# Kernel optimization log

Measured on AMD Instinct MI355X. Metric: run time of the kernel, lower is better.

The kernel has to match this reference:

```python
import jax, jax.numpy as jnp
import numpy as np

C = 1.0          # Poincare ball curvature
H = 8            # num_heads
EPS = 1e-15
DELTA = 1e-7
SC = np.sqrt(C)  # sqrt curvature


def _norm(x):
    return jnp.sqrt(jnp.clip(jnp.sum(x * x, -1, keepdims=True), 1e-15))


def mobius_add(x, y):
    xy = jnp.sum(x * y, -1, keepdims=True)
    x2 = jnp.sum(x * x, -1, keepdims=True)
    y2 = jnp.sum(y * y, -1, keepdims=True)
    num = (1 + 2 * C * xy + C * y2) * x + (1 - C * x2) * y
    den = 1 + 2 * C * xy + C * C * x2 * y2
    return num / (den + EPS)


def mobius_matvec(W, x):
    xn = _norm(x)
    mx = x @ W.T
    mxn = _norm(mx)
    arg = jnp.clip(SC * xn, None, 1 - 1e-5)
    return jnp.tanh(mxn / xn * jnp.arctanh(arg)) * mx / (mxn * SC)


def logmap0(x):
    xn = _norm(x)
    return jnp.arctanh(jnp.clip(SC * xn, None, 1 - 1e-5)) * x / (SC * xn)


def expmap0(u):
    un = _norm(u)
    return jnp.tanh(SC * un) * u / (SC * un)


def hyp_linear(W, b, x):
    return mobius_add(mobius_matvec(W, x), b)


def setup_inputs() -> dict:
    key = jax.random.key(0)
    ks = jax.random.split(key, 5)
    B, S, E = 2, 512, 256
    x = jax.random.normal(ks[0], (B, S, E), jnp.float32) * 0.02  # inside unit ball
    scale = float(np.sqrt(6.0 / (E + E)))  # xavier uniform bound
    Wq = jax.random.uniform(ks[1], (E, E), jnp.float32, -scale, scale)
    Wk = jax.random.uniform(ks[2], (E, E), jnp.float32, -scale, scale)
    Wv = jax.random.uniform(ks[3], (E, E), jnp.float32, -scale, scale)
    Wo = jax.random.uniform(ks[4], (E, E), jnp.float32, -scale, scale)
    z = jnp.zeros((E,), jnp.float32)
    head_scaling = jnp.ones((H, 1, 1), jnp.float32)
    return {"x": x, "Wq": Wq, "bq": z, "Wk": Wk, "bk": z, "Wv": Wv, "bv": z,
            "Wo": Wo, "bo": z, "head_scaling": head_scaling}


def reference(x, Wq, bq, Wk, bk, Wv, bv, Wo, bo, head_scaling):
    B, S, E = x.shape
    D = E // H
    q = hyp_linear(Wq, bq, x).reshape(B, S, H, D).transpose(0, 2, 1, 3)  # (B,H,S,D)
    k = hyp_linear(Wk, bk, x).reshape(B, S, H, D).transpose(0, 2, 1, 3)
    v = hyp_linear(Wv, bv, x).reshape(B, S, H, D).transpose(0, 2, 1, 3)
    max_norm = (1 - 1e-5) / SC
    q = jnp.minimum(q, max_norm)  # elementwise clamp_max, faithful to source
    k = jnp.minimum(k, max_norm)
    qn = C * jnp.sum(q * q, -1)[..., :, None]   # (B,H,Sq,1)
    kn = C * jnp.sum(k * k, -1)[..., None, :]   # (B,H,1,Sk)
    # pairwise mobius_add(-k, q): (B,H,Sq,Sk,D)
    diff = mobius_add(-k[:, :, None, :, :], q[:, :, :, None, :])
    dn = C * jnp.sum(diff * diff, -1)           # (B,H,Sq,Sk)
    denom = (1 - qn) * (1 - kn) + EPS
    a = jnp.maximum(1 + 2 * dn / denom, 1 + DELTA)
    dist = jnp.log(a + jnp.sqrt(a * a - 1))     # acosh
    scores = -dist / (head_scaling * np.sqrt(D))
    w = jax.nn.softmax(scores, -1)
    out = expmap0(jnp.einsum('bhqk,bhkd->bhqd', w, logmap0(v)))
    out = out.transpose(0, 2, 1, 3).reshape(B, S, E)
    return hyp_linear(Wo, bo, out)
```

## Files before the change

kernel.cpp:

```cpp
#include <hip/hip_runtime.h>
#include <math.h>

#define Ec 256
#define Sc 512
#define Bc 2
#define Hc 8
#define Dc 32
#define MAXNORM (1.0f - 1e-5f)
#define NEc (Bc * Sc * Ec)
#define KSPLIT 4
#define NROWS (Bc * Hc * Sc)

__device__ __forceinline__ float fullWaveSum(float v) {
#pragma unroll
  for (int m = 32; m >= 1; m >>= 1) v += __shfl_xor(v, m, 64);
  return v;
}
__device__ __forceinline__ float halfWaveSum(float v) {
#pragma unroll
  for (int m = 16; m >= 1; m >>= 1) v += __shfl_xor(v, m, 64);
  return v;
}
__device__ __forceinline__ float atanh_fast(float z) {
  return 0.5f * __logf((1.0f + z) / (1.0f - z));
}
__device__ __forceinline__ float tanh_fast(float a) {
  float e = __expf(-2.0f * a);
  return (1.0f - e) / (1.0f + e);
}

__global__ __launch_bounds__(128) void gemm_xwt(
    const float* __restrict__ X,
    const float* __restrict__ W0, const float* __restrict__ W1,
    const float* __restrict__ W2,
    float* __restrict__ O0, float* __restrict__ O1, float* __restrict__ O2) {
  const int tid = threadIdx.x;
  const int bx = blockIdx.x;
  const int by = blockIdx.y;
  const int kz = blockIdx.z;
  const int mat = by >> 2;
  const int cb0 = (by & 3) * 64;
  const int rb0 = bx * 32;
  const int kk = kz * 64;
  const float* __restrict__ W = (mat == 0) ? W0 : (mat == 1) ? W1 : W2;
  float* __restrict__ O = ((mat == 0) ? O0 : (mat == 1) ? O1 : O2) + (size_t)kz * NEc;

  __shared__ float Xs[64][36];
  __shared__ float Ws[64][68];

  const int f4 = tid & 15;
  const int sub = tid >> 4;
  const int ty = tid >> 4;
  const int tx = tid & 15;

#pragma unroll
  for (int i = 0; i < 4; ++i) {
    int row = sub + i * 8;
    float4 v = *(const float4*)&X[(size_t)(rb0 + row) * Ec + kk + f4 * 4];
    Xs[f4 * 4 + 0][row] = v.x;
    Xs[f4 * 4 + 1][row] = v.y;
    Xs[f4 * 4 + 2][row] = v.z;
    Xs[f4 * 4 + 3][row] = v.w;
  }
#pragma unroll
  for (int i = 0; i < 8; ++i) {
    int col = sub + i * 8;
    float4 v = *(const float4*)&W[(size_t)(cb0 + col) * Ec + kk + f4 * 4];
    Ws[f4 * 4 + 0][col] = v.x;
    Ws[f4 * 4 + 1][col] = v.y;
    Ws[f4 * 4 + 2][col] = v.z;
    Ws[f4 * 4 + 3][col] = v.w;
  }
  __syncthreads();

  float acc[4][4];
#pragma unroll
  for (int i = 0; i < 4; ++i)
#pragma unroll
    for (int j = 0; j < 4; ++j) acc[i][j] = 0.f;

#pragma unroll 8
  for (int k = 0; k < 64; ++k) {
    float4 a = *(const float4*)&Xs[k][ty * 4];
    float4 b = *(const float4*)&Ws[k][tx * 4];
    float av[4] = {a.x, a.y, a.z, a.w};
    float bv[4] = {b.x, b.y, b.z, b.w};
#pragma unroll
    for (int i = 0; i < 4; ++i)
#pragma unroll
      for (int j = 0; j < 4; ++j) acc[i][j] = fmaf(av[i], bv[j], acc[i][j]);
  }
#pragma unroll
  for (int i = 0; i < 4; ++i) {
    float4 o = make_float4(acc[i][0], acc[i][1], acc[i][2], acc[i][3]);
    *(float4*)&O[(size_t)(rb0 + ty * 4 + i) * Ec + cb0 + tx * 4] = o;
  }
}

__global__ __launch_bounds__(256) void qkv_stats(
    const float* __restrict__ x,
    const float* __restrict__ mxq, const float* __restrict__ mxk,
    const float* __restrict__ mxv,
    const float* __restrict__ bq, const float* __restrict__ bk,
    const float* __restrict__ bv,
    float* __restrict__ qo, float* __restrict__ ko, float* __restrict__ lvo,
    float* __restrict__ qno, float* __restrict__ kno) {
  const int t = threadIdx.x;
  const int row = blockIdx.x;
  const int b = row >> 9;
  const int s = row & (Sc - 1);
  const size_t idx = (size_t)row * Ec + t;
  const float xv = x[idx];
  float mq = 0.f, mk = 0.f, mv = 0.f;
#pragma unroll
  for (int p = 0; p < KSPLIT; ++p) {
    mq += mxq[idx + (size_t)p * NEc];
    mk += mxk[idx + (size_t)p * NEc];
    mv += mxv[idx + (size_t)p * NEc];
  }
  const float bb[3] = {bq[t], bk[t], bv[t]};
  const float mvals[3] = {mq, mk, mv};

  float vals[10] = {xv * xv,
                    mq * mq, mq * bb[0], bb[0] * bb[0],
                    mk * mk, mk * bb[1], bb[1] * bb[1],
                    mv * mv, mv * bb[2], bb[2] * bb[2]};
  __shared__ float red[10][4];
  __shared__ float fin[10];
#pragma unroll
  for (int i = 0; i < 10; ++i) {
    float v = fullWaveSum(vals[i]);
    if ((t & 63) == 0) red[i][t >> 6] = v;
  }
  __syncthreads();
  if (t < 10) fin[t] = red[t][0] + red[t][1] + red[t][2] + red[t][3];
  __syncthreads();

  const float x2 = fin[0];
  const float xn = sqrtf(fmaxf(x2, 1e-15f));
  const float at = atanh_fast(fminf(xn, MAXNORM));
  const int h = t >> 5;

#pragma unroll
  for (int m = 0; m < 3; ++m) {
    float mx2 = fin[1 + 3 * m];
    float mxb = fin[2 + 3 * m];
    float b2 = fin[3 + 3 * m];
    float mxn = sqrtf(fmaxf(mx2, 1e-15f));
    float scl = tanh_fast((mxn / xn) * at) / mxn;
    float mvv = scl * mvals[m];
    float X2 = scl * scl * mx2;
    float XY = scl * mxb;
    float numc = 1.0f + 2.0f * XY + b2;
    float den = 1.0f + 2.0f * XY + X2 * b2 + 1e-15f;
    float res = (numc * mvv + (1.0f - X2) * bb[m]) / den;
    if (m < 2) {
      res = fminf(res, MAXNORM);
      float s2 = halfWaveSum(res * res);
      if (m == 0) {
        qo[idx] = res;
        if ((t & 31) == 0) qno[(b * Hc + h) * Sc + s] = s2;
      } else {
        ko[idx] = res;
        if ((t & 31) == 0) kno[(b * Hc + h) * Sc + s] = s2;
      }
    } else {
      float vn2 = halfWaveSum(res * res);
      float vn = sqrtf(fmaxf(vn2, 1e-15f));
      float f = atanh_fast(fminf(vn, MAXNORM)) / vn;
      lvo[idx] = f * res;
    }
  }
}

__global__ __launch_bounds__(256) void score_kernel(
    const float* __restrict__ q, const float* __restrict__ k,
    const float* __restrict__ qn, const float* __restrict__ kn,
    const float* __restrict__ hs, float* __restrict__ P) {
  const int tid = threadIdx.x;
  const int sk0 = blockIdx.x * 64;
  const int sq0 = blockIdx.y * 64;
  const int bh = blockIdx.z;
  const int b = bh >> 3;
  const int h = bh & 7;

  __shared__ float Qs[64][32];
  __shared__ float Ks[64][32];

#pragma unroll
  for (int i = 0; i < 2; ++i) {
    int qi = tid + i * 256;
    int r = qi >> 3;
    int fd = qi & 7;
    int fsw = fd ^ ((r >> 2) & 7);
    float4 v = *(const float4*)&q[(size_t)(b * Sc + sq0 + r) * Ec + h * Dc + fd * 4];
    *(float4*)&Qs[r][fsw * 4] = v;
    float4 w = *(const float4*)&k[(size_t)(b * Sc + sk0 + r) * Ec + h * Dc + fd * 4];
    *(float4*)&Ks[r][fsw * 4] = w;
  }
  __syncthreads();

  const int ty = tid >> 4;
  const int tx = tid & 15;

  float acc[4][4];
#pragma unroll
  for (int i = 0; i < 4; ++i)
#pragma unroll
    for (int j = 0; j < 4; ++j) acc[i][j] = 0.f;

#pragma unroll
  for (int fd = 0; fd < 8; ++fd) {
    const int qsw = (fd ^ (ty & 7)) * 4;
    const int ksw = (fd ^ (tx & 7)) * 4;
    float4 a[4], bb[4];
#pragma unroll
    for (int i = 0; i < 4; ++i) a[i] = *(const float4*)&Qs[ty * 4 + i][qsw];
#pragma unroll
    for (int j = 0; j < 4; ++j) bb[j] = *(const float4*)&Ks[tx * 4 + j][ksw];
#pragma unroll
    for (int i = 0; i < 4; ++i)
#pragma unroll
      for (int j = 0; j < 4; ++j) {
        acc[i][j] = fmaf(a[i].x, bb[j].x, acc[i][j]);
        acc[i][j] = fmaf(a[i].y, bb[j].y, acc[i][j]);
        acc[i][j] = fmaf(a[i].z, bb[j].z, acc[i][j]);
        acc[i][j] = fmaf(a[i].w, bb[j].w, acc[i][j]);
      }
  }

  const float sinv = -1.0f / (hs[h] * sqrtf((float)Dc));
  float qnv[4], knv[4];
#pragma unroll
  for (int i = 0; i < 4; ++i) qnv[i] = qn[bh * Sc + sq0 + ty * 4 + i];
#pragma unroll
  for (int j = 0; j < 4; ++j) knv[j] = kn[bh * Sc + sk0 + tx * 4 + j];

#pragma unroll
  for (int i = 0; i < 4; ++i) {
    const float q2 = qnv[i];
    const float omq = 1.0f - q2;
    float4 o;
    float po[4];
#pragma unroll
    for (int j = 0; j < 4; ++j) {
      const float k2 = knv[j];
      const float kq = acc[i][j];
      const float omk = 1.0f - k2;
      float s2x2 = fmaf(-4.0f, kq, 2.0f * k2 + 2.0f * q2);
      float dden = fmaf(k2, q2, fmaf(-2.0f, kq, 1.0f)) + 1e-15f;
      float Pd = fmaf(dden, omk * omq, 1e-20f);
      float rp = __builtin_amdgcn_rcpf(Pd);
      float tt = fmaxf(s2x2 * rp, 1e-7f);
      float z = (1.0f + tt) + sqrtf(fmaf(tt, tt, tt + tt));
      po[j] = __expf(sinv * __logf(z));
    }
    o.x = po[0]; o.y = po[1]; o.z = po[2]; o.w = po[3];
    *(float4*)&P[((size_t)bh * Sc + sq0 + ty * 4 + i) * Sc + sk0 + tx * 4] = o;
  }
}

__global__ __launch_bounds__(256) void pv_kernel(
    const float* __restrict__ P, const float* __restrict__ lv,
    float* __restrict__ out) {
  const int tid = threadIdx.x;
  const int sq0 = blockIdx.x * 32;
  const int bh = blockIdx.y;
  const int b = bh >> 3;
  const int h = bh & 7;
  const int r = tid >> 3;
  const int dq = tid & 7;

  __shared__ float Ps[32][68];
  __shared__ float lvs[64][36];

  float4 acc = make_float4(0.f, 0.f, 0.f, 0.f);
  float lsum = 0.f;

#pragma unroll 1
  for (int t = 0; t < 8; ++t) {
    const int j0 = t * 64;
#pragma unroll
    for (int i = 0; i < 2; ++i) {
      int qi = tid + i * 256;
      int pr = qi >> 4, pc = qi & 15;
      *(float4*)&Ps[pr][pc * 4] =
          *(const float4*)&P[((size_t)bh * Sc + sq0 + pr) * Sc + j0 + pc * 4];
      int lr = qi >> 3, lc = qi & 7;
      *(float4*)&lvs[lr][lc * 4] =
          *(const float4*)&lv[(size_t)(b * Sc + j0 + lr) * Ec + h * Dc + lc * 4];
    }
    __syncthreads();

#pragma unroll
    for (int j4 = 0; j4 < 16; ++j4) {
      float4 pv = *(const float4*)&Ps[r][j4 * 4];
      float4 l0 = *(const float4*)&lvs[j4 * 4 + 0][dq * 4];
      float4 l1 = *(const float4*)&lvs[j4 * 4 + 1][dq * 4];
      float4 l2 = *(const float4*)&lvs[j4 * 4 + 2][dq * 4];
      float4 l3 = *(const float4*)&lvs[j4 * 4 + 3][dq * 4];
      acc.x = fmaf(pv.x, l0.x, acc.x); acc.y = fmaf(pv.x, l0.y, acc.y);
      acc.z = fmaf(pv.x, l0.z, acc.z); acc.w = fmaf(pv.x, l0.w, acc.w);
      acc.x = fmaf(pv.y, l1.x, acc.x); acc.y = fmaf(pv.y, l1.y, acc.y);
      acc.z = fmaf(pv.y, l1.z, acc.z); acc.w = fmaf(pv.y, l1.w, acc.w);
      acc.x = fmaf(pv.z, l2.x, acc.x); acc.y = fmaf(pv.z, l2.y, acc.y);
      acc.z = fmaf(pv.z, l2.z, acc.z); acc.w = fmaf(pv.z, l2.w, acc.w);
      acc.x = fmaf(pv.w, l3.x, acc.x); acc.y = fmaf(pv.w, l3.y, acc.y);
      acc.z = fmaf(pv.w, l3.z, acc.z); acc.w = fmaf(pv.w, l3.w, acc.w);
      lsum += pv.x + pv.y + pv.z + pv.w;
    }
    __syncthreads();
  }

  const float li = 1.0f / lsum;
  float o[4] = {acc.x * li, acc.y * li, acc.z * li, acc.w * li};
  float un2 = fmaf(o[0], o[0], fmaf(o[1], o[1], fmaf(o[2], o[2], o[3] * o[3])));
#pragma unroll
  for (int m = 4; m >= 1; m >>= 1) un2 += __shfl_xor(un2, m, 8);
  float un = sqrtf(fmaxf(un2, 1e-15f));
  float f = tanh_fast(un) / un;
  float4 ov = make_float4(o[0] * f, o[1] * f, o[2] * f, o[3] * f);
  *(float4*)&out[(size_t)(b * Sc + sq0 + r) * Ec + h * Dc + dq * 4] = ov;
}

__global__ __launch_bounds__(256) void proj_stats(
    const float* __restrict__ xin, const float* __restrict__ mx,
    const float* __restrict__ bo, float* __restrict__ out) {
  const int t = threadIdx.x;
  const int row = blockIdx.x;
  const size_t idx = (size_t)row * Ec + t;
  const float xv = xin[idx];
  float m = 0.f;
#pragma unroll
  for (int p = 0; p < KSPLIT; ++p) m += mx[idx + (size_t)p * NEc];
  const float bb = bo[t];
  float vals[4] = {xv * xv, m * m, m * bb, bb * bb};
  __shared__ float red[4][4];
  __shared__ float fin[4];
#pragma unroll
  for (int i = 0; i < 4; ++i) {
    float v = fullWaveSum(vals[i]);
    if ((t & 63) == 0) red[i][t >> 6] = v;
  }
  __syncthreads();
  if (t < 4) fin[t] = red[t][0] + red[t][1] + red[t][2] + red[t][3];
  __syncthreads();

  float x2 = fin[0], mx2 = fin[1], mxb = fin[2], b2 = fin[3];
  float xn = sqrtf(fmaxf(x2, 1e-15f));
  float mxn = sqrtf(fmaxf(mx2, 1e-15f));
  float scl = tanh_fast((mxn / xn) * atanh_fast(fminf(xn, MAXNORM))) / mxn;
  float mvv = scl * m;
  float X2 = scl * scl * mx2;
  float XY = scl * mxb;
  float numc = 1.0f + 2.0f * XY + b2;
  float den = 1.0f + 2.0f * XY + X2 * b2 + 1e-15f;
  out[idx] = (numc * mvv + (1.0f - X2) * bb) / den;
}

extern "C" void kernel_launch(void* const* d_in, const int* in_sizes, int n_in,
                              void* d_out, int out_size, void* d_ws, size_t ws_size,
                              hipStream_t stream) {
  (void)in_sizes; (void)n_in; (void)out_size; (void)ws_size;
  const float* x  = (const float*)d_in[0];
  const float* Wq = (const float*)d_in[1];
  const float* bq = (const float*)d_in[2];
  const float* Wk = (const float*)d_in[3];
  const float* bk = (const float*)d_in[4];
  const float* Wv = (const float*)d_in[5];
  const float* bv = (const float*)d_in[6];
  const float* Wo = (const float*)d_in[7];
  const float* bo = (const float*)d_in[8];
  const float* hs = (const float*)d_in[9];

  float* ws = (float*)d_ws;
  const int NE = NEc;
  const int NH = NROWS;
  float* mxq = ws;
  float* mxk = mxq + KSPLIT * NE;
  float* mxv = mxk + KSPLIT * NE;
  float* mxo = mxv + KSPLIT * NE;
  float* qb  = mxo + KSPLIT * NE;
  float* kb  = qb + NE;
  float* lvb = kb + NE;
  float* aob = lvb + NE;
  float* qnb = aob + NE;
  float* knb = qnb + NH;
  float* Pb  = knb + NH;

  const int M = Bc * Sc;

  gemm_xwt<<<dim3(M / 32, 12, KSPLIT), 128, 0, stream>>>(x, Wq, Wk, Wv, mxq, mxk, mxv);
  qkv_stats<<<M, 256, 0, stream>>>(x, mxq, mxk, mxv, bq, bk, bv,
                                   qb, kb, lvb, qnb, knb);
  score_kernel<<<dim3(8, 8, 16), 256, 0, stream>>>(qb, kb, qnb, knb, hs, Pb);
  pv_kernel<<<dim3(16, 16), 256, 0, stream>>>(Pb, lvb, aob);
  gemm_xwt<<<dim3(M / 32, 4, KSPLIT), 128, 0, stream>>>(aob, Wo, Wo, Wo, mxo, mxo, mxo);
  proj_stats<<<M, 256, 0, stream>>>(aob, mxo, bo, (float*)d_out);
}
```

Baseline: 137.0 us.

## Split PV reduction over key chunks with register tiling and shared-memory combine

The PV kernel now handles 16 query rows per block, giving twice as many blocks. Each thread accumulates a 4-row by 4-column register tile over its own 8-key slice of every 64-key chunk, and partial sums are combined through shared memory before normalisation and expmap. This targets low occupancy in pv_kernel (only 256 blocks) and gives more reuse of each LDS load. The cost is extra shared memory, one more barrier and a reduction step. Separately, the score kernel swaps __expf/__logf for the raw exp2/log2 intrinsics, which skips the base conversions and is valid only if sinv already carries the log2 scaling.

```diff
diff --git a/kernel.cpp b/kernel.cpp
--- a/kernel.cpp
+++ b/kernel.cpp
@@ -253,7 +253,7 @@
       float rp = __builtin_amdgcn_rcpf(Pd);
       float tt = fmaxf(s2x2 * rp, 1e-7f);
       float z = (1.0f + tt) + sqrtf(fmaf(tt, tt, tt + tt));
-      po[j] = __expf(sinv * __logf(z));
+      po[j] = __builtin_amdgcn_exp2f(sinv * __builtin_amdgcn_logf(z));
     }
     o.x = po[0]; o.y = po[1]; o.z = po[2]; o.w = po[3];
     *(float4*)&P[((size_t)bh * Sc + sq0 + ty * 4 + i) * Sc + sk0 + tx * 4] = o;
@@ -264,63 +264,102 @@
     const float* __restrict__ P, const float* __restrict__ lv,
     float* __restrict__ out) {
   const int tid = threadIdx.x;
-  const int sq0 = blockIdx.x * 32;
+  const int sq0 = blockIdx.x * 16;
   const int bh = blockIdx.y;
   const int b = bh >> 3;
   const int h = bh & 7;
-  const int r = tid >> 3;
+  const int js = tid >> 5;
+  const int rg = (tid >> 3) & 3;
   const int dq = tid & 7;
 
-  __shared__ float Ps[32][68];
+  __shared__ float Ps[16][68];
   __shared__ float lvs[64][36];
-
-  float4 acc = make_float4(0.f, 0.f, 0.f, 0.f);
-  float lsum = 0.f;
+  __shared__ float accm[16][8][32];
+  __shared__ float lsb[16][9];
+
+  float4 acc[4];
+#pragma unroll
+  for (int i = 0; i < 4; ++i) acc[i] = make_float4(0.f, 0.f, 0.f, 0.f);
+  float lsum4[4] = {0.f, 0.f, 0.f, 0.f};
 
 #pragma unroll 1
   for (int t = 0; t < 8; ++t) {
-    const int j0 = t * 64;
-#pragma unroll
-    for (int i = 0; i < 2; ++i) {
-      int qi = tid + i * 256;
-      int pr = qi >> 4, pc = qi & 15;
+    const int j0g = t * 64;
+    {
+      int pr = tid >> 4, pc = tid & 15;
       *(float4*)&Ps[pr][pc * 4] =
-          *(const float4*)&P[((size_t)bh * Sc + sq0 + pr) * Sc + j0 + pc * 4];
-      int lr = qi >> 3, lc = qi & 7;
-      *(float4*)&lvs[lr][lc * 4] =
-          *(const float4*)&lv[(size_t)(b * Sc + j0 + lr) * Ec + h * Dc + lc * 4];
+          *(const float4*)&P[((size_t)bh * Sc + sq0 + pr) * Sc + j0g + pc * 4];
+#pragma unroll
+      for (int i = 0; i < 2; ++i) {
+        int qi = tid + i * 256;
+        int lr = qi >> 3, lc = qi & 7;
+        *(float4*)&lvs[lr][lc * 4] =
+            *(const float4*)&lv[(size_t)(b * Sc + j0g + lr) * Ec + h * Dc + lc * 4];
+      }
     }
     __syncthreads();
 
 #pragma unroll
-    for (int j4 = 0; j4 < 16; ++j4) {
-      float4 pv = *(const float4*)&Ps[r][j4 * 4];
-      float4 l0 = *(const float4*)&lvs[j4 * 4 + 0][dq * 4];
-      float4 l1 = *(const float4*)&lvs[j4 * 4 + 1][dq * 4];
-      float4 l2 = *(const float4*)&lvs[j4 * 4 + 2][dq * 4];
-      float4 l3 = *(const float4*)&lvs[j4 * 4 + 3][dq * 4];
-      acc.x = fmaf(pv.x, l0.x, acc.x); acc.y = fmaf(pv.x, l0.y, acc.y);
-      acc.z = fmaf(pv.x, l0.z, acc.z); acc.w = fmaf(pv.x, l0.w, acc.w);
-      acc.x = fmaf(pv.y, l1.x, acc.x); acc.y = fmaf(pv.y, l1.y, acc.y);
-      acc.z = fmaf(pv.y, l1.z, acc.z); acc.w = fmaf(pv.y, l1.w, acc.w);
-      acc.x = fmaf(pv.z, l2.x, acc.x); acc.y = fmaf(pv.z, l2.y, acc.y);
-      acc.z = fmaf(pv.z, l2.z, acc.z); acc.w = fmaf(pv.z, l2.w, acc.w);
-      acc.x = fmaf(pv.w, l3.x, acc.x); acc.y = fmaf(pv.w, l3.y, acc.y);
-      acc.z = fmaf(pv.w, l3.z, acc.z); acc.w = fmaf(pv.w, l3.w, acc.w);
-      lsum += pv.x + pv.y + pv.z + pv.w;
+    for (int j4 = 0; j4 < 2; ++j4) {
+      const int j0 = js * 8 + j4 * 4;
+      float4 p[4], l[4];
+#pragma unroll
+      for (int i = 0; i < 4; ++i) p[i] = *(const float4*)&Ps[rg * 4 + i][j0];
+#pragma unroll
+      for (int c = 0; c < 4; ++c) l[c] = *(const float4*)&lvs[j0 + c][dq * 4];
+#pragma unroll
+      for (int i = 0; i < 4; ++i) {
+        lsum4[i] += (p[i].x + p[i].y) + (p[i].z + p[i].w);
+        acc[i].x = fmaf(p[i].x, l[0].x, acc[i].x);
+        acc[i].y = fmaf(p[i].x, l[0].y, acc[i].y);
+        acc[i].z = fmaf(p[i].x, l[0].z, acc[i].z);
+        acc[i].w = fmaf(p[i].x, l[0].w, acc[i].w);
+        acc[i].x = fmaf(p[i].y, l[1].x, acc[i].x);
+        acc[i].y = fmaf(p[i].y, l[1].y, acc[i].y);
+        acc[i].z = fmaf(p[i].y, l[1].z, acc[i].z);
+        acc[i].w = fmaf(p[i].y, l[1].w, acc[i].w);
+        acc[i].x = fmaf(p[i].z, l[2].x, acc[i].x);
+        acc[i].y = fmaf(p[i].z, l[2].y, acc[i].y);
+        acc[i].z = fmaf(p[i].z, l[2].z, acc[i].z);
+        acc[i].w = fmaf(p[i].z, l[2].w, acc[i].w);
+        acc[i].x = fmaf(p[i].w, l[3].x, acc[i].x);
+        acc[i].y = fmaf(p[i].w, l[3].y, acc[i].y);
+        acc[i].z = fmaf(p[i].w, l[3].z, acc[i].z);
+        acc[i].w = fmaf(p[i].w, l[3].w, acc[i].w);
+      }
     }
     __syncthreads();
   }
 
-  const float li = 1.0f / lsum;
-  float o[4] = {acc.x * li, acc.y * li, acc.z * li, acc.w * li};
-  float un2 = fmaf(o[0], o[0], fmaf(o[1], o[1], fmaf(o[2], o[2], o[3] * o[3])));
-#pragma unroll
-  for (int m = 4; m >= 1; m >>= 1) un2 += __shfl_xor(un2, m, 8);
+#pragma unroll
+  for (int i = 0; i < 4; ++i)
+    *(float4*)&accm[rg * 4 + i][js][dq * 4] = acc[i];
+  if (dq == 0) {
+#pragma unroll
+    for (int i = 0; i < 4; ++i) lsb[rg * 4 + i][js] = lsum4[i];
+  }
+  __syncthreads();
+
+  const int r2 = tid >> 4;
+  const int dd = tid & 15;
+  float o0 = 0.f, o1 = 0.f, ls = 0.f;
+#pragma unroll
+  for (int g = 0; g < 8; ++g) {
+    float2 a2 = *(const float2*)&accm[r2][g][dd * 2];
+    o0 += a2.x;
+    o1 += a2.y;
+    ls += lsb[r2][g];
+  }
+  const float li = 1.0f / ls;
+  o0 *= li;
+  o1 *= li;
+  float un2 = fmaf(o0, o0, o1 * o1);
+#pragma unroll
+  for (int m = 8; m >= 1; m >>= 1) un2 += __shfl_xor(un2, m, 16);
   float un = sqrtf(fmaxf(un2, 1e-15f));
   float f = tanh_fast(un) / un;
-  float4 ov = make_float4(o[0] * f, o[1] * f, o[2] * f, o[3] * f);
-  *(float4*)&out[(size_t)(b * Sc + sq0 + r) * Ec + h * Dc + dq * 4] = ov;
+  float2 ov = make_float2(o0 * f, o1 * f);
+  *(float2*)&out[(size_t)(b * Sc + sq0 + r2) * Ec + h * Dc + dd * 2] = ov;
 }
 
 __global__ __launch_bounds__(256) void proj_stats(
@@ -394,7 +433,7 @@
   qkv_stats<<<M, 256, 0, stream>>>(x, mxq, mxk, mxv, bq, bk, bv,
                                    qb, kb, lvb, qnb, knb);
   score_kernel<<<dim3(8, 8, 16), 256, 0, stream>>>(qb, kb, qnb, knb, hs, Pb);
-  pv_kernel<<<dim3(16, 16), 256, 0, stream>>>(Pb, lvb, aob);
+  pv_kernel<<<dim3(32, 16), 256, 0, stream>>>(Pb, lvb, aob);
   gemm_xwt<<<dim3(M / 32, 4, KSPLIT), 128, 0, stream>>>(aob, Wo, Wo, Wo, mxo, mxo, mxo);
   proj_stats<<<M, 256, 0, stream>>>(aob, mxo, bo, (float*)d_out);
 }
```

Measured after the change: 125.0 us. 1.1x faster.
